# Optimization experiments

Measured on AMD Instinct MI355X. Metric: run time of the kernel, lower is better.

## Reference

```python
import jax, jax.numpy as jnp
import numpy as np

B, C, H, W = 16, 128, 56, 56
QK, HEADS, NWIN, TOPK, MLPR = 128, 4, 7, 4, 3
HD_Q, HD_V = QK // HEADS, C // HEADS
WH, WW = H // NWIN, W // NWIN          # 8, 8 tokens per window side
P2, W2 = NWIN * NWIN, WH * WW          # 49 regions, 64 tokens/region
SCALE = QK ** -0.5                     # BiFormer uses full qk_dim**-0.5 for both router and pixel attn


def _dwconv(x, w, b):
    # x: (B,C,H,W); w: (C,1,k,k) depthwise, odd k with SAME padding == torch padding=k//2
    y = jax.lax.conv_general_dilated(x, w, (1, 1), 'SAME',
                                     feature_group_count=x.shape[1],
                                     dimension_numbers=('NCHW', 'OIHW', 'NCHW'))
    return y + b[None, :, None, None]


def _ln(x, g, b):
    m = x.mean(-1, keepdims=True)
    v = ((x - m) ** 2).mean(-1, keepdims=True)
    return (x - m) * jax.lax.rsqrt(v + 1e-6) * g + b


def _win(t):  # (B,H,W,c) -> (B,P2,WH,WW,c)
    b, _, _, c = t.shape
    return t.reshape(b, NWIN, WH, NWIN, WW, c).transpose(0, 1, 3, 2, 4, 5).reshape(b, P2, WH, WW, c)


def _unwin(t):  # (B,P2,W2,c) -> (B,H,W,c)
    b, c = t.shape[0], t.shape[-1]
    return t.reshape(b, NWIN, NWIN, WH, WW, c).transpose(0, 1, 3, 2, 4, 5).reshape(b, H, W, c)


def setup_inputs() -> dict:
    key = jax.random.key(0)
    ks = jax.random.split(key, 8)
    p = lambda k, sh: (0.02 * jax.random.normal(k, sh)).astype(jnp.float32)
    return {
        'x': jax.random.normal(ks[0], (B, C, H, W), dtype=jnp.float32),
        'pos_w': p(ks[1], (C, 1, 3, 3)), 'pos_b': jnp.zeros((C,), jnp.float32),
        'ln1_g': jnp.ones((C,), jnp.float32), 'ln1_b': jnp.zeros((C,), jnp.float32),
        'qkv_w': p(ks[2], (C, 2 * QK + C)), 'qkv_b': jnp.zeros((2 * QK + C,), jnp.float32),
        'lepe_w': p(ks[3], (C, 1, 5, 5)), 'lepe_b': jnp.zeros((C,), jnp.float32),
        'wo_w': p(ks[4], (C, C)), 'wo_b': jnp.zeros((C,), jnp.float32),
        'ln2_g': jnp.ones((C,), jnp.float32), 'ln2_b': jnp.zeros((C,), jnp.float32),
        'mlp_w1': p(ks[5], (C, MLPR * C)), 'mlp_b1': jnp.zeros((MLPR * C,), jnp.float32),
        'mlp_w2': p(ks[6], (MLPR * C, C)), 'mlp_b2': jnp.zeros((C,), jnp.float32),
    }


def reference(x, pos_w, pos_b, ln1_g, ln1_b, qkv_w, qkv_b, lepe_w, lepe_b,
              wo_w, wo_b, ln2_g, ln2_b, mlp_w1, mlp_b1, mlp_w2, mlp_b2):
    # CPE: x = x + depthwise3x3(x)
    x = x + _dwconv(x, pos_w, pos_b)
    xh = x.transpose(0, 2, 3, 1)                        # NHWC

    # ---- BiLevelRoutingAttention(norm1(x)) ----
    y = _ln(xh, ln1_g, ln1_b)
    qkv = y @ qkv_w + qkv_b                             # (B,H,W,2*QK+C)
    q, kv = qkv[..., :QK], qkv[..., QK:]                # kv = [k | v]
    qw, kvw = _win(q), _win(kv)                         # (B,P2,WH,WW,.)

    # region-level routing: detached window means, coarse affinity, top-k regions
    q_win = jax.lax.stop_gradient(qw.mean((2, 3)))      # (B,P2,QK)
    k_win = jax.lax.stop_gradient(kvw[..., :QK].mean((2, 3)))
    logits = jnp.einsum('bpc,bqc->bpq', q_win * SCALE, k_win)
    _, idx = jax.lax.top_k(logits, TOPK)                # (B,P2,TOPK) int32

    # gather k/v tokens of the selected regions (mul_weight='none': weights unused)
    kv_pix = kvw.reshape(B, P2, W2, QK + C)
    kv_sel = jax.vmap(lambda t, i: t[i])(kv_pix, idx)   # (B,P2,TOPK,W2,QK+C)
    k_sel = kv_sel[..., :QK].reshape(B, P2, TOPK * W2, HEADS, HD_Q)
    v_sel = kv_sel[..., QK:].reshape(B, P2, TOPK * W2, HEADS, HD_V)
    q_pix = qw.reshape(B, P2, W2, HEADS, HD_Q)

    att = jnp.einsum('bpqhd,bpkhd->bphqk', q_pix * SCALE, k_sel)
    att = jax.nn.softmax(att, axis=-1)
    o = jnp.einsum('bphqk,bpkhd->bpqhd', att, v_sel).reshape(B, P2, W2, C)
    o = _unwin(o)                                       # (B,H,W,C)

    # LePE: depthwise 5x5 on v over the full image, then output projection
    v_img = kv[..., QK:].transpose(0, 3, 1, 2)
    lepe = _dwconv(v_img, lepe_w, lepe_b).transpose(0, 2, 3, 1)
    o = (o + lepe) @ wo_w + wo_b
    xh = xh + o

    # ---- MLP(norm2(x)) ----
    z = _ln(xh, ln2_g, ln2_b)
    z = jax.nn.gelu(z @ mlp_w1 + mlp_b1, approximate=False) @ mlp_w2 + mlp_b2
    xh = xh + z
    return xh.transpose(0, 3, 1, 2)                     # back to NCHW
```

## Files before the change

### kernel.cpp

```cpp
#include <hip/hip_runtime.h>
#include <math.h>

#define BATCH 16
#define CH    128
#define HGT   56
#define WID   56
#define NPIX  (BATCH*HGT*WID)
#define NQKV  384
#define NWIN  7
#define P2    49
#define TOPK  4
#define ATT_SCALE 0.088388347648318447f

typedef __attribute__((ext_vector_type(8))) short short8;
typedef __attribute__((ext_vector_type(4))) short short4v;
typedef __attribute__((ext_vector_type(4))) float float4v;

static __device__ __forceinline__ unsigned short f2bf(float f) {
  unsigned u = __float_as_uint(f);
  u += 0x7fffu + ((u >> 16) & 1u);
  return (unsigned short)(u >> 16);
}
static __device__ __forceinline__ float bf2f(unsigned short u) {
  return __uint_as_float((unsigned)u << 16);
}

__global__ __launch_bounds__(128) void k_prep(
    const float* __restrict__ qkv_w, const float* __restrict__ wo_w,
    const float* __restrict__ mlp_w1, const float* __restrict__ mlp_w2,
    unsigned short* __restrict__ Wq, unsigned short* __restrict__ Wo,
    unsigned short* __restrict__ W1, unsigned short* __restrict__ W2) {
  int bx = blockIdx.x, t = threadIdx.x;
  if (bx < 384) {
    int n = bx;
    Wq[n*128 + t] = f2bf(qkv_w[(size_t)t*384 + n]);
  } else if (bx < 512) {
    int n = bx - 384;
    Wo[n*128 + t] = f2bf(wo_w[(size_t)t*128 + n]);
  } else if (bx < 896) {
    int n = bx - 512;
    W1[n*128 + t] = f2bf(mlp_w1[(size_t)t*384 + n]);
  } else {
    int n = bx - 896;
    for (int k = t; k < 384; k += 128)
      W2[n*384 + k] = f2bf(mlp_w2[(size_t)k*128 + n]);
  }
}

__global__ __launch_bounds__(256) void k_posconv(const float* __restrict__ x,
    const float* __restrict__ pw, const float* __restrict__ pb,
    float* __restrict__ xh) {
  __shared__ float sh[10*58*32];
  int b = blockIdx.y;
  int rg = blockIdx.x >> 2, cg = blockIdx.x & 3;
  int row0 = rg*8, c0 = cg*32;
  int t = threadIdx.x;
  for (int i = t; i < 10*58*32/4; i += 256)
    ((int4*)sh)[i] = make_int4(0,0,0,0);
  __syncthreads();
  for (int i = t; i < 4480; i += 256) {
    int c = i & 31, chunk = (i >> 5) % 14, rr = i / 448;
    int grow = row0 + rr - 1;
    if ((unsigned)grow < HGT) {
      float4 v = *(const float4*)(x + ((size_t)(b*CH + c0 + c))*(HGT*WID)
                                  + grow*WID + chunk*4);
      float* d = &sh[(rr*58 + 1 + chunk*4)*32 + c];
      d[0] = v.x; d[32] = v.y; d[64] = v.z; d[96] = v.w;
    }
  }
  __syncthreads();
  int c = t & 31, pg = t >> 5;
  float w[9];
#pragma unroll
  for (int i = 0; i < 9; i++) w[i] = pw[(c0 + c)*9 + i];
  float bias = pb[c0 + c];
  const float* rowp[3];
#pragma unroll
  for (int dy = 0; dy < 3; dy++) rowp[dy] = &sh[((pg + dy)*58)*32 + c];
  float win[3][3];
#pragma unroll
  for (int j = 0; j < 2; j++)
#pragma unroll
    for (int dy = 0; dy < 3; dy++) win[j][dy] = rowp[dy][j*32];
  float* ob = &xh[(((size_t)b*HGT + row0 + pg)*WID)*CH + c0 + c];
#pragma unroll
  for (int col = 0; col < 56; col++) {
    int slot = (col + 2) % 3;
#pragma unroll
    for (int dy = 0; dy < 3; dy++) win[slot][dy] = rowp[dy][(col + 2)*32];
    float s = bias + win[(col + 1) % 3][1];
#pragma unroll
    for (int dx = 0; dx < 3; dx++) {
      int sl = (col + dx) % 3;
#pragma unroll
      for (int dy = 0; dy < 3; dy++) s += win[sl][dy] * w[dy*3 + dx];
    }
    ob[col*CH] = s;
  }
}

__global__ __launch_bounds__(256) void k_route(const float* __restrict__ xh,
    const float* __restrict__ g, const float* __restrict__ be,
    const float* __restrict__ qkv_w, const float* __restrict__ qkv_b,
    float* __restrict__ qwin, float* __restrict__ kwin) {
  __shared__ float yt[128*68];
  __shared__ float ym[128];
  int bp = blockIdx.x; int b = bp / P2, p = bp % P2;
  int wy = p / NWIN, wx = p % NWIN;
  int t = threadIdx.x;
  int pl = t >> 2, qu = t & 3;
  {
    int hg = wy*8 + (pl >> 3), wg = wx*8 + (pl & 7);
    const float4* src = (const float4*)(xh + (((size_t)b*HGT + hg)*WID + wg)*CH + qu*32);
    float v[32]; float s = 0.f, ss = 0.f;
#pragma unroll
    for (int i = 0; i < 8; i++) {
      float4 f = src[i];
      v[4*i] = f.x; v[4*i+1] = f.y; v[4*i+2] = f.z; v[4*i+3] = f.w;
      s += f.x + f.y + f.z + f.w;
      ss += f.x*f.x + f.y*f.y + f.z*f.z + f.w*f.w;
    }
    s += __shfl_xor(s, 1); ss += __shfl_xor(ss, 1);
    s += __shfl_xor(s, 2); ss += __shfl_xor(ss, 2);
    float m  = s * (1.f/128.f);
    float var = ss * (1.f/128.f) - m*m;
    float rs = rsqrtf(var + 1e-6f);
#pragma unroll
    for (int i = 0; i < 32; i++) {
      int ch = qu*32 + i;
      yt[ch*68 + pl] = (v[i] - m) * rs * g[ch] + be[ch];
    }
  }
  __syncthreads();
  if (t < 128) {
    const float4* col = (const float4*)&yt[t*68];
    float4 a = make_float4(0.f,0.f,0.f,0.f);
#pragma unroll
    for (int i = 0; i < 16; i++) {
      float4 f = col[i];
      a.x += f.x; a.y += f.y; a.z += f.z; a.w += f.w;
    }
    ym[t] = (a.x + a.y + a.z + a.w) * (1.f/64.f);
  }
  __syncthreads();
  {
    int n = t;
    float s = qkv_b[n];
#pragma unroll 4
    for (int c = 0; c < 128; c++) s += ym[c] * qkv_w[(size_t)c*NQKV + n];
    if (n < 128) qwin[(size_t)bp*128 + n] = s;
    else         kwin[(size_t)bp*128 + n - 128] = s;
  }
}

__global__ __launch_bounds__(256) void k_topk(const float* __restrict__ qwin,
    const float* __restrict__ kwin, int* __restrict__ idx) {
  __shared__ float logits[64];
  int bp = blockIdx.x; int b = bp / P2;
  int t = threadIdx.x;
  int key = t >> 2, qu = t & 3;
  float s = 0.f;
  if (key < P2) {
    const float4* qp = (const float4*)(qwin + (size_t)bp*128 + qu*32);
    const float4* kp = (const float4*)(kwin + ((size_t)b*P2 + key)*128 + qu*32);
#pragma unroll
    for (int i = 0; i < 8; i++) {
      float4 qv = qp[i], kv = kp[i];
      s += qv.x*kv.x + qv.y*kv.y + qv.z*kv.z + qv.w*kv.w;
    }
  }
  s += __shfl_xor(s, 1);
  s += __shfl_xor(s, 2);
  if (qu == 0 && key < P2) logits[key] = s;
  __syncthreads();
  if (t == 0) {
    unsigned long long used = 0ULL;
    for (int tt = 0; tt < TOPK; tt++) {
      float best = -1e30f; int bi = 0;
      for (int q = 0; q < P2; q++) {
        bool ok = !((used >> q) & 1ULL);
        float lv = logits[q];
        if (ok && lv > best) { best = lv; bi = q; }
      }
      used |= 1ULL << bi;
      idx[(size_t)bp*TOPK + tt] = bi;
    }
  }
}

__global__ __launch_bounds__(256, 2) void k_qkv_gemm(
    const float* __restrict__ in, const float* __restrict__ g,
    const float* __restrict__ be, const unsigned short* __restrict__ Wt,
    const float* __restrict__ bias,
    unsigned short* __restrict__ qW, unsigned short* __restrict__ kW,
    unsigned short* __restrict__ vT) {
  __shared__ __align__(16) unsigned short aL[128*136];
  __shared__ __align__(16) unsigned short bL[128*136];
  int base = blockIdx.x * 128;
  int t = threadIdx.x;
  {
    int r = t >> 1, half = t & 1;
    const float4* src = (const float4*)(in + (size_t)(base + r)*CH + half*64);
    float v[64];
    float s = 0.f, ss = 0.f;
#pragma unroll
    for (int i = 0; i < 16; i++) {
      float4 f = src[i];
      v[4*i] = f.x; v[4*i+1] = f.y; v[4*i+2] = f.z; v[4*i+3] = f.w;
      s += f.x + f.y + f.z + f.w;
      ss += f.x*f.x + f.y*f.y + f.z*f.z + f.w*f.w;
    }
    s += __shfl_xor(s, 1); ss += __shfl_xor(ss, 1);
    float m  = s * (1.f/128.f);
    float var = ss * (1.f/128.f) - m*m;
    float rs = rsqrtf(var + 1e-6f);
    union { unsigned short us[8]; int4 v4; } pk;
#pragma unroll
    for (int c8 = 0; c8 < 8; c8++) {
#pragma unroll
      for (int j = 0; j < 8; j++) {
        int ch = half*64 + c8*8 + j;
        pk.us[j] = f2bf((v[c8*8 + j] - m) * rs * g[ch] + be[ch]);
      }
      *(int4*)&aL[r*136 + half*64 + c8*8] = pk.v4;
    }
  }
  int wid = t >> 6, lane = t & 63;
  int ln = lane & 15, q = lane >> 4;
  int wr = (wid >> 1)*64, wc = (wid & 1)*64;
  for (int chunk = 0; chunk < 3; chunk++) {
    if (chunk) __syncthreads();
    for (int i = t; i < 2048; i += 256) {
      int row = i >> 4, seg = i & 15;
      *(int4*)&bL[row*136 + seg*8] =
          *(const int4*)(Wt + (size_t)(chunk*128 + row)*128 + seg*8);
    }
    __syncthreads();
    float4v acc[4][4];
#pragma unroll
    for (int a = 0; a < 4; a++)
#pragma unroll
      for (int b2 = 0; b2 < 4; b2++)
        acc[a][b2] = (float4v){0.f, 0.f, 0.f, 0.f};
#pragma unroll
    for (int kk = 0; kk < 4; kk++) {
      int ko = kk*32 + q*8;
      short8 af[4], bf[4];
#pragma unroll
      for (int mf = 0; mf < 4; mf++)
        af[mf] = *(const short8*)&aL[(wr + mf*16 + ln)*136 + ko];
#pragma unroll
      for (int nf = 0; nf < 4; nf++)
        bf[nf] = *(const short8*)&bL[(wc + nf*16 + ln)*136 + ko];
#pragma unroll
      for (int mf = 0; mf < 4; mf++)
#pragma unroll
        for (int nf = 0; nf < 4; nf++)
          acc[mf][nf] = __builtin_amdgcn_mfma_f32_16x16x32_bf16(
              af[mf], bf[nf], acc[mf][nf], 0, 0, 0);
    }
    if (chunk < 2) {
      unsigned short* dst = chunk ? kW : qW;
      float sc = chunk ? 1.f : ATT_SCALE;
#pragma unroll
      for (int mf = 0; mf < 4; mf++) {
#pragma unroll
        for (int j = 0; j < 4; j++) {
          int pg = base + wr + mf*16 + q*4 + j;
          int b  = pg / 3136, sp = pg - b*3136;
          int hh = sp / 56, ww = sp - hh*56;
          int p  = (hh >> 3)*NWIN + (ww >> 3);
          int ploc = (hh & 7)*8 + (ww & 7);
          size_t rb = ((size_t)(b*P2 + p)*64 + ploc)*128;
#pragma unroll
          for (int nf = 0; nf < 4; nf++) {
            int col = wc + nf*16 + ln;
            dst[rb + col] = f2bf((acc[mf][nf][j] + bias[chunk*128 + col])*sc);
          }
        }
      }
    } else {
      __syncthreads();
#pragma unroll
      for (int mf = 0; mf < 4; mf++)
#pragma unroll
        for (int nf = 0; nf < 4; nf++) {
          int row = wr + mf*16 + q*4;
          int col = wc + nf*16 + ln;
          float b4 = bias[256 + col];
          short4v pk;
#pragma unroll
          for (int j = 0; j < 4; j++) pk[j] = (short)f2bf(acc[mf][nf][j] + b4);
          *(short4v*)&bL[col*136 + row] = pk;
        }
      __syncthreads();
      int c = t >> 1, half = t & 1;
#pragma unroll
      for (int g8 = 0; g8 < 8; g8++) {
        int pg0 = base + half*64 + g8*8;
        int b = pg0 / 3136, sp = pg0 - b*3136;
        *(int4*)(vT + ((size_t)(b*CH + c))*3136 + sp) =
            *(int4*)&bL[c*136 + half*64 + g8*8];
      }
    }
  }
}

#define PLS 72
__global__ __launch_bounds__(256) void k_attn_mfma(
    const unsigned short* __restrict__ qW, const unsigned short* __restrict__ kW,
    const unsigned short* __restrict__ vT, const int* __restrict__ idx,
    float* __restrict__ o) {
  __shared__ unsigned short pL[4][64*PLS];
  int bx = blockIdx.x;
  int b = bx & 15, p = bx >> 4;
  int bp = b*P2 + p;
  int wy = p / NWIN, wx = p % NWIN;
  int h = threadIdx.x >> 6, lane = threadIdx.x & 63;
  int ln = lane & 15, q = lane >> 4;

  short8 aq[4];
#pragma unroll
  for (int mf = 0; mf < 4; mf++)
    aq[mf] = *(const short8*)&qW[((size_t)bp*64 + mf*16 + ln)*128 + h*32 + q*8];

  int4 widx = *(const int4*)&idx[(size_t)bp*TOPK];
  int wins[4] = {widx.x, widx.y, widx.z, widx.w};

  float l_run[4][4];
  float4v facc[4][2];
#pragma unroll
  for (int mf = 0; mf < 4; mf++) {
#pragma unroll
    for (int j = 0; j < 4; j++) l_run[mf][j] = 0.f;
    facc[mf][0] = (float4v){0.f,0.f,0.f,0.f};
    facc[mf][1] = (float4v){0.f,0.f,0.f,0.f};
  }

  unsigned short* myP = &pL[h][0];
  int swr = ((ln >> 2) & 3) * 16;

  for (int r = 0; r < TOPK; r++) {
    int win = wins[r];
    int sy = win / NWIN, sx = win % NWIN;
    short8 bk[4];
#pragma unroll
    for (int nf = 0; nf < 4; nf++)
      bk[nf] = *(const short8*)&kW[(((size_t)b*P2 + win)*64 + nf*16 + ln)*128 + h*32 + q*8];
    float4v sacc[4][4];
#pragma unroll
    for (int mf = 0; mf < 4; mf++)
#pragma unroll
      for (int nf = 0; nf < 4; nf++)
        sacc[mf][nf] = (float4v){0.f,0.f,0.f,0.f};
#pragma unroll
    for (int mf = 0; mf < 4; mf++)
#pragma unroll
      for (int nf = 0; nf < 4; nf++)
        sacc[mf][nf] = __builtin_amdgcn_mfma_f32_16x16x32_bf16(
            aq[mf], bk[nf], sacc[mf][nf], 0, 0, 0);
#pragma unroll
    for (int mf = 0; mf < 4; mf++) {
#pragma unroll
      for (int j = 0; j < 4; j++) {
        float e0 = __expf(sacc[mf][0][j]);
        float e1 = __expf(sacc[mf][1][j]);
        float e2 = __expf(sacc[mf][2][j]);
        float e3 = __expf(sacc[mf][3][j]);
        l_run[mf][j] += (e0 + e1) + (e2 + e3);
        int rowoff = (mf*16 + q*4 + j)*PLS;
        int sww = q*16;
        myP[rowoff + (( 0 + ln) ^ sww)] = f2bf(e0);
        myP[rowoff + ((16 + ln) ^ sww)] = f2bf(e1);
        myP[rowoff + ((32 + ln) ^ sww)] = f2bf(e2);
        myP[rowoff + ((48 + ln) ^ sww)] = f2bf(e3);
      }
    }
#pragma unroll
    for (int kk = 0; kk < 2; kk++) {
      short8 ap[4];
#pragma unroll
      for (int mf = 0; mf < 4; mf++)
        ap[mf] = *(const short8*)&myP[(mf*16 + ln)*PLS + ((kk*32 + q*8) ^ swr)];
      short8 bv[2];
#pragma unroll
      for (int nf2 = 0; nf2 < 2; nf2++) {
        int d = h*32 + nf2*16 + ln;
        int K0 = kk*32 + q*8;
        const unsigned short* vp = vT + ((size_t)b*CH + d)*(HGT*WID)
            + (sy*8 + (K0 >> 3))*WID + sx*8;
        bv[nf2] = *(const short8*)vp;
      }
#pragma unroll
      for (int mf = 0; mf < 4; mf++)
#pragma unroll
        for (int nf2 = 0; nf2 < 2; nf2++)
          facc[mf][nf2] = __builtin_amdgcn_mfma_f32_16x16x32_bf16(
              ap[mf], bv[nf2], facc[mf][nf2], 0, 0, 0);
    }
  }
#pragma unroll
  for (int mf = 0; mf < 4; mf++)
#pragma unroll
    for (int j = 0; j < 4; j++) {
      float l = l_run[mf][j];
      l += __shfl_xor(l, 1);
      l += __shfl_xor(l, 2);
      l += __shfl_xor(l, 4);
      l += __shfl_xor(l, 8);
      float inv = 1.f / l;
      int prow = mf*16 + q*4 + j;
      size_t pg = ((size_t)b*HGT + wy*8 + (prow>>3))*WID + wx*8 + (prow&7);
      o[pg*CH + h*32 + ln]      = facc[mf][0][j] * inv;
      o[pg*CH + h*32 + 16 + ln] = facc[mf][1][j] * inv;
    }
}

__global__ __launch_bounds__(256) void k_lepe(const unsigned short* __restrict__ vT,
    const float* __restrict__ lw, const float* __restrict__ lb,
    float* __restrict__ o) {
  __shared__ unsigned short sh[12*60*32];
  int b = blockIdx.y;
  int rg = blockIdx.x >> 2, cg = blockIdx.x & 3;
  int row0 = rg*8, c0 = cg*32;
  int t = threadIdx.x;
  for (int i = t; i < 12*60*32/8; i += 256)
    ((int4*)sh)[i] = make_int4(0,0,0,0);
  __syncthreads();
  for (int i = t; i < 2688; i += 256) {
    int chunk = i % 7, rr = (i/7) % 12, c = i / 84;
    int grow = row0 + rr - 2;
    if ((unsigned)grow < HGT) {
      int4 v = *(const int4*)(vT + ((size_t)(b*CH + c0 + c))*(HGT*WID) + grow*WID + chunk*8);
      union { int4 v4; unsigned short us[8]; } u; u.v4 = v;
#pragma unroll
      for (int j = 0; j < 8; j++)
        sh[(rr*60 + 2 + chunk*8 + j)*32 + c] = u.us[j];
    }
  }
  __syncthreads();
  int c = t & 31, pg = t >> 5;
  float w[25];
#pragma unroll
  for (int i = 0; i < 25; i++) w[i] = lw[(c0 + c)*25 + i];
  float bias = lb[c0 + c];
  const unsigned short* rowp[5];
#pragma unroll
  for (int dy = 0; dy < 5; dy++) rowp[dy] = &sh[((pg + dy)*60)*32 + c];
  float win[5][5];
#pragma unroll
  for (int j = 0; j < 4; j++)
#pragma unroll
    for (int dy = 0; dy < 5; dy++) win[j][dy] = bf2f(rowp[dy][j*32]);
  float* ob = &o[(((size_t)b*HGT + row0 + pg)*WID)*CH + c0 + c];
#pragma unroll
  for (int col = 0; col < 56; col++) {
    int slot = (col + 4) % 5;
#pragma unroll
    for (int dy = 0; dy < 5; dy++) win[slot][dy] = bf2f(rowp[dy][(col + 4)*32]);
    float s = bias;
#pragma unroll
    for (int dx = 0; dx < 5; dx++) {
      int sl = (col + dx) % 5;
#pragma unroll
      for (int dy = 0; dy < 5; dy++) s += win[sl][dy] * w[dy*5 + dx];
    }
    ob[col*CH] += s;
  }
}

__global__ __launch_bounds__(256, 2) void k_wo_mfma(
    const float* __restrict__ in, const unsigned short* __restrict__ Wt,
    const float* __restrict__ bias, float* __restrict__ xh) {
  __shared__ __align__(16) unsigned short aL[128*136];
  __shared__ __align__(16) unsigned short bL[128*136];
  size_t base = (size_t)blockIdx.x * 128;
  int t = threadIdx.x;
  {
    int r = t >> 1, half = t & 1;
    const float4* src = (const float4*)(in + (base + r)*CH + half*64);
    union { unsigned short us[8]; int4 v4; } pk;
#pragma unroll
    for (int c8 = 0; c8 < 8; c8++) {
      float4 f0 = src[c8*2], f1 = src[c8*2 + 1];
      pk.us[0] = f2bf(f0.x); pk.us[1] = f2bf(f0.y);
      pk.us[2] = f2bf(f0.z); pk.us[3] = f2bf(f0.w);
      pk.us[4] = f2bf(f1.x); pk.us[5] = f2bf(f1.y);
      pk.us[6] = f2bf(f1.z); pk.us[7] = f2bf(f1.w);
      *(int4*)&aL[r*136 + half*64 + c8*8] = pk.v4;
    }
  }
  for (int i = t; i < 2048; i += 256) {
    int row = i >> 4, seg = i & 15;
    *(int4*)&bL[row*136 + seg*8] = *(const int4*)(Wt + (size_t)row*128 + seg*8);
  }
  __syncthreads();
  int wid = t >> 6, lane = t & 63;
  int ln = lane & 15, q = lane >> 4;
  int wr = (wid >> 1)*64, wc = (wid & 1)*64;
  float4v acc[4][4];
#pragma unroll
  for (int a = 0; a < 4; a++)
#pragma unroll
    for (int b = 0; b < 4; b++)
      acc[a][b] = (float4v){0.f, 0.f, 0.f, 0.f};
#pragma unroll
  for (int kk = 0; kk < 4; kk++) {
    int ko = kk*32 + q*8;
    short8 af[4], bf[4];
#pragma unroll
    for (int mf = 0; mf < 4; mf++)
      af[mf] = *(const short8*)&aL[(wr + mf*16 + ln)*136 + ko];
#pragma unroll
    for (int nf = 0; nf < 4; nf++)
      bf[nf] = *(const short8*)&bL[(wc + nf*16 + ln)*136 + ko];
#pragma unroll
    for (int mf = 0; mf < 4; mf++)
#pragma unroll
      for (int nf = 0; nf < 4; nf++)
        acc[mf][nf] = __builtin_amdgcn_mfma_f32_16x16x32_bf16(
            af[mf], bf[nf], acc[mf][nf], 0, 0, 0);
  }
#pragma unroll
  for (int mf = 0; mf < 4; mf++)
#pragma unroll
    for (int nf = 0; nf < 4; nf++) {
      int row = wr + mf*16 + q*4;
      int col = wc + nf*16 + ln;
      float b4 = bias[col];
#pragma unroll
      for (int j = 0; j < 4; j++) {
        float* p = &xh[(base + row + j)*CH + col];
        *p += acc[mf][nf][j] + b4;
      }
    }
}

__global__ __launch_bounds__(256, 2) void k_mlp1_gemm(
    const float* __restrict__ in, const float* __restrict__ g,
    const float* __restrict__ be, const unsigned short* __restrict__ Wt,
    const float* __restrict__ bias, unsigned short* __restrict__ hidb) {
  __shared__ __align__(16) unsigned short aL[128*136];
  __shared__ __align__(16) unsigned short bL[128*136];
  size_t base = (size_t)blockIdx.x * 128;
  int t = threadIdx.x;
  {
    int r = t >> 1, half = t & 1;
    const float4* src = (const float4*)(in + (base + r)*CH + half*64);
    float v[64];
    float s = 0.f, ss = 0.f;
#pragma unroll
    for (int i = 0; i < 16; i++) {
      float4 f = src[i];
      v[4*i] = f.x; v[4*i+1] = f.y; v[4*i+2] = f.z; v[4*i+3] = f.w;
      s += f.x + f.y + f.z + f.w;
      ss += f.x*f.x + f.y*f.y + f.z*f.z + f.w*f.w;
    }
    s += __shfl_xor(s, 1); ss += __shfl_xor(ss, 1);
    float m  = s * (1.f/128.f);
    float var = ss * (1.f/128.f) - m*m;
    float rs = rsqrtf(var + 1e-6f);
    union { unsigned short us[8]; int4 v4; } pk;
#pragma unroll
    for (int c8 = 0; c8 < 8; c8++) {
#pragma unroll
      for (int j = 0; j < 8; j++) {
        int ch = half*64 + c8*8 + j;
        pk.us[j] = f2bf((v[c8*8 + j] - m) * rs * g[ch] + be[ch]);
      }
      *(int4*)&aL[r*136 + half*64 + c8*8] = pk.v4;
    }
  }
  int wid = t >> 6, lane = t & 63;
  int ln = lane & 15, q = lane >> 4;
  int wr = (wid >> 1)*64, wc = (wid & 1)*64;
  for (int chunk = 0; chunk < 3; chunk++) {
    if (chunk) __syncthreads();
    for (int i = t; i < 2048; i += 256) {
      int row = i >> 4, seg = i & 15;
      *(int4*)&bL[row*136 + seg*8] =
          *(const int4*)(Wt + (size_t)(chunk*128 + row)*128 + seg*8);
    }
    __syncthreads();
    float4v acc[4][4];
#pragma unroll
    for (int a = 0; a < 4; a++)
#pragma unroll
      for (int b = 0; b < 4; b++)
        acc[a][b] = (float4v){0.f, 0.f, 0.f, 0.f};
#pragma unroll
    for (int kk = 0; kk < 4; kk++) {
      int ko = kk*32 + q*8;
      short8 af[4], bf[4];
#pragma unroll
      for (int mf = 0; mf < 4; mf++)
        af[mf] = *(const short8*)&aL[(wr + mf*16 + ln)*136 + ko];
#pragma unroll
      for (int nf = 0; nf < 4; nf++)
        bf[nf] = *(const short8*)&bL[(wc + nf*16 + ln)*136 + ko];
#pragma unroll
      for (int mf = 0; mf < 4; mf++)
#pragma unroll
        for (int nf = 0; nf < 4; nf++)
          acc[mf][nf] = __builtin_amdgcn_mfma_f32_16x16x32_bf16(
              af[mf], bf[nf], acc[mf][nf], 0, 0, 0);
    }
#pragma unroll
    for (int mf = 0; mf < 4; mf++)
#pragma unroll
      for (int nf = 0; nf < 4; nf++) {
        int row = wr + mf*16 + q*4;
        int col = wc + nf*16 + ln + chunk*128;
        float b4 = bias[col];
#pragma unroll
        for (int j = 0; j < 4; j++) {
          float vv = acc[mf][nf][j] + b4;
          vv = 0.5f * vv * (1.f + erff(vv * 0.70710678118654752f));
          hidb[(base + row + j)*NQKV + col] = f2bf(vv);
        }
      }
  }
}

__global__ __launch_bounds__(256, 2) void k_mlp2_mfma(
    const unsigned short* __restrict__ hidb, const unsigned short* __restrict__ Wt,
    const float* __restrict__ bias, const float* __restrict__ xh,
    float* __restrict__ out) {
  __shared__ __align__(16) unsigned short aL[128*136];
  __shared__ __align__(16) unsigned short bL[128*136];
  size_t base = (size_t)blockIdx.x * 128;
  int t = threadIdx.x;
  int wid = t >> 6, lane = t & 63;
  int ln = lane & 15, q = lane >> 4;
  int wr = (wid >> 1)*64, wc = (wid & 1)*64;
  float4v acc[4][4];
#pragma unroll
  for (int a = 0; a < 4; a++)
#pragma unroll
    for (int b = 0; b < 4; b++)
      acc[a][b] = (float4v){0.f, 0.f, 0.f, 0.f};
  for (int kc = 0; kc < 3; kc++) {
    if (kc) __syncthreads();
    {
      int r = t >> 1, half = t & 1;
      const int4* src = (const int4*)(hidb + (base + r)*NQKV + kc*128 + half*64);
#pragma unroll
      for (int i = 0; i < 8; i++)
        *(int4*)&aL[r*136 + half*64 + i*8] = src[i];
    }
    for (int i = t; i < 2048; i += 256) {
      int row = i >> 4, seg = i & 15;
      *(int4*)&bL[row*136 + seg*8] =
          *(const int4*)(Wt + (size_t)row*NQKV + kc*128 + seg*8);
    }
    __syncthreads();
#pragma unroll
    for (int kk = 0; kk < 4; kk++) {
      int ko = kk*32 + q*8;
      short8 af[4], bf[4];
#pragma unroll
      for (int mf = 0; mf < 4; mf++)
        af[mf] = *(const short8*)&aL[(wr + mf*16 + ln)*136 + ko];
#pragma unroll
      for (int nf = 0; nf < 4; nf++)
        bf[nf] = *(const short8*)&bL[(wc + nf*16 + ln)*136 + ko];
#pragma unroll
      for (int mf = 0; mf < 4; mf++)
#pragma unroll
        for (int nf = 0; nf < 4; nf++)
          acc[mf][nf] = __builtin_amdgcn_mfma_f32_16x16x32_bf16(
              af[mf], bf[nf], acc[mf][nf], 0, 0, 0);
    }
  }
#pragma unroll
  for (int mf = 0; mf < 4; mf++)
#pragma unroll
    for (int nf = 0; nf < 4; nf++) {
      int row = wr + mf*16 + q*4;
      int col = wc + nf*16 + ln;
      float b4 = bias[col];
#pragma unroll
      for (int j = 0; j < 4; j++) {
        size_t pixel = base + row + j;
        int b = (int)(pixel / (HGT*WID));
        int sp = (int)(pixel % (HGT*WID));
        out[((size_t)b*CH + col)*(HGT*WID) + sp] =
            acc[mf][nf][j] + b4 + xh[pixel*CH + col];
      }
    }
}

extern "C" void kernel_launch(void* const* d_in, const int* in_sizes, int n_in,
                              void* d_out, int out_size, void* d_ws, size_t ws_size,
                              hipStream_t stream) {
  const float* x      = (const float*)d_in[0];
  const float* pos_w  = (const float*)d_in[1];
  const float* pos_b  = (const float*)d_in[2];
  const float* ln1_g  = (const float*)d_in[3];
  const float* ln1_b  = (const float*)d_in[4];
  const float* qkv_w  = (const float*)d_in[5];
  const float* qkv_b  = (const float*)d_in[6];
  const float* lepe_w = (const float*)d_in[7];
  const float* lepe_b = (const float*)d_in[8];
  const float* wo_w   = (const float*)d_in[9];
  const float* wo_b   = (const float*)d_in[10];
  const float* ln2_g  = (const float*)d_in[11];
  const float* ln2_b  = (const float*)d_in[12];
  const float* mlp_w1 = (const float*)d_in[13];
  const float* mlp_b1 = (const float*)d_in[14];
  const float* mlp_w2 = (const float*)d_in[15];
  const float* mlp_b2 = (const float*)d_in[16];

  float* ws   = (float*)d_ws;
  float* xh   = ws;
  float* o    = xh + (size_t)NPIX*CH;
  float* qwin = o  + (size_t)NPIX*CH;
  float* kwin = qwin + (size_t)BATCH*P2*128;
  int*   idx  = (int*)(kwin + (size_t)BATCH*P2*128);
  unsigned short* Wq = (unsigned short*)(idx + BATCH*P2*TOPK);
  unsigned short* Wo = Wq + 384*128;
  unsigned short* W1 = Wo + 128*128;
  unsigned short* W2 = W1 + 384*128;
  unsigned short* vT = W2 + 128*384;
  unsigned short* qW = vT + (size_t)NPIX*CH;
  unsigned short* kW = qW + (size_t)NPIX*CH;
  unsigned short* hidb = kW + (size_t)NPIX*CH;

  k_prep<<<1024, 128, 0, stream>>>(qkv_w, wo_w, mlp_w1, mlp_w2, Wq, Wo, W1, W2);
  k_posconv<<<dim3(28, BATCH), 256, 0, stream>>>(x, pos_w, pos_b, xh);
  k_route<<<BATCH*P2, 256, 0, stream>>>(xh, ln1_g, ln1_b, qkv_w, qkv_b, qwin, kwin);
  k_topk<<<BATCH*P2, 256, 0, stream>>>(qwin, kwin, idx);
  k_qkv_gemm<<<NPIX/128, 256, 0, stream>>>(xh, ln1_g, ln1_b, Wq, qkv_b, qW, kW, vT);
  k_attn_mfma<<<BATCH*P2, 256, 0, stream>>>(qW, kW, vT, idx, o);
  k_lepe<<<dim3(28, BATCH), 256, 0, stream>>>(vT, lepe_w, lepe_b, o);
  k_wo_mfma<<<NPIX/128, 256, 0, stream>>>(o, Wo, wo_b, xh);
  k_mlp1_gemm<<<NPIX/128, 256, 0, stream>>>(xh, ln2_g, ln2_b, W1, mlp_b1, hidb);
  k_mlp2_mfma<<<NPIX/128, 256, 0, stream>>>(hidb, W2, mlp_b2, xh, (float*)d_out);
}
```

Baseline: 327.7 us.

## Load GEMM operands directly from global memory instead of LDS staging

In the four projection/MLP GEMM kernels, the LDS staging of the weight tile (and for the Wo and MLP2 kernels also the activation tile) is removed, and MFMA fragments are read straight from global memory. The Wo kernel converts fp32 activations to bf16 in registers per fragment. Freeing LDS and raising the launch-bounds occupancy hint from 2 to 4 blocks per CU aims to drop barriers and staging copies and rely on L1/L2 caching. The cost is that each operand is now fetched redundantly by several waves through strided, uncoalesced 16-byte global loads.

```diff
diff --git a/kernel.cpp b/kernel.cpp
--- a/kernel.cpp
+++ b/kernel.cpp
@@ -23,6 +23,12 @@
 }
 static __device__ __forceinline__ float bf2f(unsigned short u) {
   return __uint_as_float((unsigned)u << 16);
+}
+static __device__ __forceinline__ short8 cvt8(float4 a, float4 b) {
+  union { unsigned short us[8]; short8 s8; } u;
+  u.us[0] = f2bf(a.x); u.us[1] = f2bf(a.y); u.us[2] = f2bf(a.z); u.us[3] = f2bf(a.w);
+  u.us[4] = f2bf(b.x); u.us[5] = f2bf(b.y); u.us[6] = f2bf(b.z); u.us[7] = f2bf(b.w);
+  return u.s8;
 }
 
 __global__ __launch_bounds__(128) void k_prep(
@@ -188,14 +194,13 @@
   }
 }
 
-__global__ __launch_bounds__(256, 2) void k_qkv_gemm(
+__global__ __launch_bounds__(256, 4) void k_qkv_gemm(
     const float* __restrict__ in, const float* __restrict__ g,
     const float* __restrict__ be, const unsigned short* __restrict__ Wt,
     const float* __restrict__ bias,
     unsigned short* __restrict__ qW, unsigned short* __restrict__ kW,
     unsigned short* __restrict__ vT) {
   __shared__ __align__(16) unsigned short aL[128*136];
-  __shared__ __align__(16) unsigned short bL[128*136];
   int base = blockIdx.x * 128;
   int t = threadIdx.x;
   {
@@ -225,17 +230,11 @@
       *(int4*)&aL[r*136 + half*64 + c8*8] = pk.v4;
     }
   }
+  __syncthreads();
   int wid = t >> 6, lane = t & 63;
   int ln = lane & 15, q = lane >> 4;
   int wr = (wid >> 1)*64, wc = (wid & 1)*64;
   for (int chunk = 0; chunk < 3; chunk++) {
-    if (chunk) __syncthreads();
-    for (int i = t; i < 2048; i += 256) {
-      int row = i >> 4, seg = i & 15;
-      *(int4*)&bL[row*136 + seg*8] =
-          *(const int4*)(Wt + (size_t)(chunk*128 + row)*128 + seg*8);
-    }
-    __syncthreads();
     float4v acc[4][4];
 #pragma unroll
     for (int a = 0; a < 4; a++)
@@ -251,7 +250,7 @@
         af[mf] = *(const short8*)&aL[(wr + mf*16 + ln)*136 + ko];
 #pragma unroll
       for (int nf = 0; nf < 4; nf++)
-        bf[nf] = *(const short8*)&bL[(wc + nf*16 + ln)*136 + ko];
+        bf[nf] = *(const short8*)&Wt[(size_t)(chunk*128 + wc + nf*16 + ln)*128 + ko];
 #pragma unroll
       for (int mf = 0; mf < 4; mf++)
 #pragma unroll
@@ -291,7 +290,7 @@
           short4v pk;
 #pragma unroll
           for (int j = 0; j < 4; j++) pk[j] = (short)f2bf(acc[mf][nf][j] + b4);
-          *(short4v*)&bL[col*136 + row] = pk;
+          *(short4v*)&aL[col*136 + row] = pk;
         }
       __syncthreads();
       int c = t >> 1, half = t & 1;
@@ -300,7 +299,7 @@
         int pg0 = base + half*64 + g8*8;
         int b = pg0 / 3136, sp = pg0 - b*3136;
         *(int4*)(vT + ((size_t)(b*CH + c))*3136 + sp) =
-            *(int4*)&bL[c*136 + half*64 + g8*8];
+            *(int4*)&aL[c*136 + half*64 + g8*8];
       }
     }
   }
@@ -469,32 +468,11 @@
   }
 }
 
-__global__ __launch_bounds__(256, 2) void k_wo_mfma(
+__global__ __launch_bounds__(256, 4) void k_wo_mfma(
     const float* __restrict__ in, const unsigned short* __restrict__ Wt,
     const float* __restrict__ bias, float* __restrict__ xh) {
-  __shared__ __align__(16) unsigned short aL[128*136];
-  __shared__ __align__(16) unsigned short bL[128*136];
   size_t base = (size_t)blockIdx.x * 128;
   int t = threadIdx.x;
-  {
-    int r = t >> 1, half = t & 1;
-    const float4* src = (const float4*)(in + (base + r)*CH + half*64);
-    union { unsigned short us[8]; int4 v4; } pk;
-#pragma unroll
-    for (int c8 = 0; c8 < 8; c8++) {
-      float4 f0 = src[c8*2], f1 = src[c8*2 + 1];
-      pk.us[0] = f2bf(f0.x); pk.us[1] = f2bf(f0.y);
-      pk.us[2] = f2bf(f0.z); pk.us[3] = f2bf(f0.w);
-      pk.us[4] = f2bf(f1.x); pk.us[5] = f2bf(f1.y);
-      pk.us[6] = f2bf(f1.z); pk.us[7] = f2bf(f1.w);
-      *(int4*)&aL[r*136 + half*64 + c8*8] = pk.v4;
-    }
-  }
-  for (int i = t; i < 2048; i += 256) {
-    int row = i >> 4, seg = i & 15;
-    *(int4*)&bL[row*136 + seg*8] = *(const int4*)(Wt + (size_t)row*128 + seg*8);
-  }
-  __syncthreads();
   int wid = t >> 6, lane = t & 63;
   int ln = lane & 15, q = lane >> 4;
   int wr = (wid >> 1)*64, wc = (wid & 1)*64;
@@ -509,11 +487,13 @@
     int ko = kk*32 + q*8;
     short8 af[4], bf[4];
 #pragma unroll
-    for (int mf = 0; mf < 4; mf++)
-      af[mf] = *(const short8*)&aL[(wr + mf*16 + ln)*136 + ko];
+    for (int mf = 0; mf < 4; mf++) {
+      const float* ap = in + (base + wr + mf*16 + ln)*CH + ko;
+      af[mf] = cvt8(*(const float4*)ap, *(const float4*)(ap + 4));
+    }
 #pragma unroll
     for (int nf = 0; nf < 4; nf++)
-      bf[nf] = *(const short8*)&bL[(wc + nf*16 + ln)*136 + ko];
+      bf[nf] = *(const short8*)&Wt[(size_t)(wc + nf*16 + ln)*128 + ko];
 #pragma unroll
     for (int mf = 0; mf < 4; mf++)
 #pragma unroll
@@ -536,12 +516,11 @@
     }
 }
 
-__global__ __launch_bounds__(256, 2) void k_mlp1_gemm(
+__global__ __launch_bounds__(256, 4) void k_mlp1_gemm(
     const float* __restrict__ in, const float* __restrict__ g,
     const float* __restrict__ be, const unsigned short* __restrict__ Wt,
     const float* __restrict__ bias, unsigned short* __restrict__ hidb) {
   __shared__ __align__(16) unsigned short aL[128*136];
-  __shared__ __align__(16) unsigned short bL[128*136];
   size_t base = (size_t)blockIdx.x * 128;
   int t = threadIdx.x;
   {
@@ -571,17 +550,11 @@
       *(int4*)&aL[r*136 + half*64 + c8*8] = pk.v4;
     }
   }
+  __syncthreads();
   int wid = t >> 6, lane = t & 63;
   int ln = lane & 15, q = lane >> 4;
   int wr = (wid >> 1)*64, wc = (wid & 1)*64;
   for (int chunk = 0; chunk < 3; chunk++) {
-    if (chunk) __syncthreads();
-    for (int i = t; i < 2048; i += 256) {
-      int row = i >> 4, seg = i & 15;
-      *(int4*)&bL[row*136 + seg*8] =
-          *(const int4*)(Wt + (size_t)(chunk*128 + row)*128 + seg*8);
-    }
-    __syncthreads();
     float4v acc[4][4];
 #pragma unroll
     for (int a = 0; a < 4; a++)
@@ -597,7 +570,7 @@
         af[mf] = *(const short8*)&aL[(wr + mf*16 + ln)*136 + ko];
 #pragma unroll
       for (int nf = 0; nf < 4; nf++)
-        bf[nf] = *(const short8*)&bL[(wc + nf*16 + ln)*136 + ko];
+        bf[nf] = *(const short8*)&Wt[(size_t)(chunk*128 + wc + nf*16 + ln)*128 + ko];
 #pragma unroll
       for (int mf = 0; mf < 4; mf++)
 #pragma unroll
@@ -622,12 +595,10 @@
   }
 }
 
-__global__ __launch_bounds__(256, 2) void k_mlp2_mfma(
+__global__ __launch_bounds__(256, 4) void k_mlp2_mfma(
     const unsigned short* __restrict__ hidb, const unsigned short* __restrict__ Wt,
     const float* __restrict__ bias, const float* __restrict__ xh,
     float* __restrict__ out) {
-  __shared__ __align__(16) unsigned short aL[128*136];
-  __shared__ __align__(16) unsigned short bL[128*136];
   size_t base = (size_t)blockIdx.x * 128;
   int t = threadIdx.x;
   int wid = t >> 6, lane = t & 63;
@@ -640,30 +611,16 @@
     for (int b = 0; b < 4; b++)
       acc[a][b] = (float4v){0.f, 0.f, 0.f, 0.f};
   for (int kc = 0; kc < 3; kc++) {
-    if (kc) __syncthreads();
-    {
-      int r = t >> 1, half = t & 1;
-      const int4* src = (const int4*)(hidb + (base + r)*NQKV + kc*128 + half*64);
-#pragma unroll
-      for (int i = 0; i < 8; i++)
-        *(int4*)&aL[r*136 + half*64 + i*8] = src[i];
-    }
-    for (int i = t; i < 2048; i += 256) {
-      int row = i >> 4, seg = i & 15;
-      *(int4*)&bL[row*136 + seg*8] =
-          *(const int4*)(Wt + (size_t)row*NQKV + kc*128 + seg*8);
-    }
-    __syncthreads();
 #pragma unroll
     for (int kk = 0; kk < 4; kk++) {
-      int ko = kk*32 + q*8;
+      int ko = kc*128 + kk*32 + q*8;
       short8 af[4], bf[4];
 #pragma unroll
       for (int mf = 0; mf < 4; mf++)
-        af[mf] = *(const short8*)&aL[(wr + mf*16 + ln)*136 + ko];
+        af[mf] = *(const short8*)&hidb[(base + wr + mf*16 + ln)*NQKV + ko];
 #pragma unroll
       for (int nf = 0; nf < 4; nf++)
-        bf[nf] = *(const short8*)&bL[(wc + nf*16 + ln)*136 + ko];
+        bf[nf] = *(const short8*)&Wt[(size_t)(wc + nf*16 + ln)*NQKV + ko];
 #pragma unroll
       for (int mf = 0; mf < 4; mf++)
 #pragma unroll
```

Result: slower. 423.8 us (+29.4%).
